# Kernel optimization log

Measured on AMD Instinct MI355X. Metric: run time of the kernel, lower is better.

Reference implementation:

```python
import jax, jax.numpy as jnp
import numpy as np

B, E, H = 16384, 1024, 1024


def setup_inputs() -> dict:
    key = jax.random.key(0)
    ks = jax.random.split(key, 8)
    s = 1.0 / np.sqrt(H)
    return {
        "x": jax.random.normal(ks[0], (B, E), dtype=jnp.float32),
        "h": jax.random.normal(ks[1], (B, H), dtype=jnp.float32),
        "W_ri": jax.random.normal(ks[2], (E, H), dtype=jnp.float32) * s,
        "b_ri": jnp.zeros((H,), dtype=jnp.float32),
        "W_rh": jax.random.normal(ks[3], (H, H), dtype=jnp.float32) * s,
        "W_zi": jax.random.normal(ks[4], (E, H), dtype=jnp.float32) * s,
        "b_zi": jnp.zeros((H,), dtype=jnp.float32),
        "W_zh": jax.random.normal(ks[5], (H, H), dtype=jnp.float32) * s,
        "W_hi": jax.random.normal(ks[6], (E, H), dtype=jnp.float32) * s,
        "b_hi": jnp.zeros((H,), dtype=jnp.float32),
        "W_hh": jax.random.normal(ks[7], (H, H), dtype=jnp.float32) * s,
    }


def reference(x, h, W_ri, b_ri, W_rh, W_zi, b_zi, W_zh, W_hi, b_hi, W_hh):
    # GRU cell: r/z gates then candidate htilde, then blend.
    rt = jax.nn.sigmoid(x @ W_ri + b_ri + h @ W_rh)          # [B,H]
    zt = jax.nn.sigmoid(x @ W_zi + b_zi + h @ W_zh)          # [B,H]
    htilde = jnp.tanh(x @ W_hi + b_hi + (h * rt) @ W_hh)     # [B,H]
    h_new = (1.0 - zt) * h + zt * htilde                     # [B,H]
    # dp_keep_prob=1.0 -> dropout is identity; module returns (dropout(h), h)
    return h_new
```

## Files before the change

### kernel.cpp

```cpp
#include <hip/hip_runtime.h>


typedef short bf16x8 __attribute__((ext_vector_type(8)));
typedef float f32x4 __attribute__((ext_vector_type(4)));

static __device__ __forceinline__ unsigned short f2bf(float f) {
    unsigned int u = __float_as_uint(f);
    return (unsigned short)((u + 0x7fffu + ((u >> 16) & 1u)) >> 16);
}
static __device__ __forceinline__ float bf2f(unsigned short s) {
    return __uint_as_float(((unsigned int)s) << 16);
}

__global__ void cast2_f32_bf16(const float* __restrict__ a,
                               const float* __restrict__ b,
                               unsigned short* __restrict__ da,
                               unsigned short* __restrict__ db, int n) {
    int i = (blockIdx.x * blockDim.x + threadIdx.x) * 4;
    const float* s;
    unsigned short* d;
    int off;
    if (i < n) { s = a; d = da; off = i; }
    else       { s = b; d = db; off = i - n; }
    float4 v = *(const float4*)(s + off);
    ushort4 o;
    o.x = f2bf(v.x); o.y = f2bf(v.y); o.z = f2bf(v.z); o.w = f2bf(v.w);
    *(ushort4*)(d + off) = o;
}

struct TPlan {
    const float* src[6];
    unsigned short* dst[6];
};
__global__ void transpose_cast6(TPlan p) {
    __shared__ float t[32][33];
    const float* src = p.src[blockIdx.z];
    unsigned short* dst = p.dst[blockIdx.z];
    int bx = blockIdx.x, by = blockIdx.y;
    int tx = threadIdx.x, ty = threadIdx.y;
#pragma unroll
    for (int i = 0; i < 4; ++i)
        t[ty + 8 * i][tx] = src[(by * 32 + ty + 8 * i) * 1024 + bx * 32 + tx];
    __syncthreads();
#pragma unroll
    for (int i = 0; i < 4; ++i) {
        int n = bx * 32 + ty + 8 * i;
        int k = by * 32 + tx;
        dst[n * 2048 + k] = f2bf(t[tx][ty + 8 * i]);
    }
}

template <int MODE, int NBN_LOG>
__global__ void gemm_gru(const unsigned short* __restrict__ Alo,
                         const unsigned short* __restrict__ Ahi,
                         const unsigned short* __restrict__ Bt,
                         const float* __restrict__ bias_z,
                         const float* __restrict__ bias_r,
                         const unsigned short* __restrict__ hb,
                         const unsigned short* __restrict__ ztb_in,
                         const float* __restrict__ hf,
                         unsigned short* __restrict__ ztb_out,
                         unsigned short* __restrict__ ab_out,
                         float* __restrict__ out) {
    constexpr int NBN = 1 << NBN_LOG;
    __shared__ __attribute__((aligned(16))) short As[128 * 32];
    __shared__ __attribute__((aligned(16))) short Bs[128 * 32];

    const int t = threadIdx.x;
    const int lane = t & 63;
    const int wave = t >> 6;
    const int i = blockIdx.x;
    const int bml = i & 7;
    const int bn = (i >> 3) & (NBN - 1);
    const int bmg = i >> (3 + NBN_LOG);
    const int bm = bmg * 8 + bml;
    const int wm = wave >> 1, wn = wave & 1;

    f32x4 acc[4][4] = {};

    const int rowA0 = bm * 128;
    const int rowB0 = bn * 128;
    const int koff = (lane >> 4) * 8;
    const int rsub = lane & 15;

    const short* Ap[4];
    const short* Bp[4];
#pragma unroll
    for (int mi = 0; mi < 4; ++mi)
        Ap[mi] = As + (wm * 64 + mi * 16 + rsub) * 32 + koff;
#pragma unroll
    for (int ni = 0; ni < 4; ++ni)
        Bp[ni] = Bs + (wn * 64 + ni * 16 + rsub) * 32 + koff;

    for (int half = 0; half < 2; ++half) {
        const unsigned short* Ab = (half ? Ahi : Alo) + rowA0 * 1024;
        const unsigned short* Bb = Bt + rowB0 * 2048 + half * 1024;
        for (int kk = 0; kk < 1024; kk += 32) {
            const unsigned short* Asrc = Ab + kk;
            const unsigned short* Bsrc = Bb + kk;

            __syncthreads();
#pragma unroll
            for (int j = 0; j < 2; ++j) {
                int c = j * 256 + wave * 64 + lane;
                int row = c >> 2, part = c & 3;
                __builtin_amdgcn_global_load_lds(
                    (const __attribute__((address_space(1))) void*)(Asrc + row * 1024 + part * 8),
                    (__attribute__((address_space(3))) void*)(As + (j * 256 + wave * 64) * 8),
                    16, 0, 0);
                __builtin_amdgcn_global_load_lds(
                    (const __attribute__((address_space(1))) void*)(Bsrc + row * 2048 + part * 8),
                    (__attribute__((address_space(3))) void*)(Bs + (j * 256 + wave * 64) * 8),
                    16, 0, 0);
            }
            __syncthreads();

            bf16x8 af[4], bfr[4];
#pragma unroll
            for (int mi = 0; mi < 4; ++mi) af[mi] = *(const bf16x8*)Ap[mi];
#pragma unroll
            for (int ni = 0; ni < 4; ++ni) bfr[ni] = *(const bf16x8*)Bp[ni];
#pragma unroll
            for (int mi = 0; mi < 4; ++mi)
#pragma unroll
                for (int ni = 0; ni < 4; ++ni)
                    acc[mi][ni] = __builtin_amdgcn_mfma_f32_16x16x32_bf16(
                        af[mi], bfr[ni], acc[mi][ni], 0, 0, 0);
        }
    }

    const int q = lane >> 4;
#pragma unroll
    for (int mi = 0; mi < 4; ++mi) {
#pragma unroll
        for (int ni = 0; ni < 4; ++ni) {
            int colg = bn * 128 + wn * 64 + ni * 16 + rsub;
            int row0 = bm * 128 + wm * 64 + mi * 16 + q * 4;
            if (MODE == 0) {
                bool isZ = colg < 1024;
                int col = colg & 1023;
                float bz = isZ ? bias_z[col] : bias_r[col];
#pragma unroll
                for (int r = 0; r < 4; ++r) {
                    int idx = (row0 + r) * 1024 + col;
                    float v = acc[mi][ni][r] + bz;
                    float s = 1.0f / (1.0f + __expf(-v));
                    if (isZ) ztb_out[idx] = f2bf(s);
                    else     ab_out[idx] = f2bf(bf2f(hb[idx]) * s);
                }
            } else {
                int col = colg;
                float bz = bias_z[col];
#pragma unroll
                for (int r = 0; r < 4; ++r) {
                    int idx = (row0 + r) * 1024 + col;
                    float v = acc[mi][ni][r] + bz;
                    float e = __expf(2.0f * v);
                    float ht = 1.0f - 2.0f / (e + 1.0f);
                    float hv = hf[idx];
                    float z = bf2f(ztb_in[idx]);
                    out[idx] = fmaf(z, ht - hv, hv);
                }
            }
        }
    }
}

extern "C" void kernel_launch(void* const* d_in, const int* in_sizes, int n_in,
                              void* d_out, int out_size, void* d_ws, size_t ws_size,
                              hipStream_t stream) {
    const float* x    = (const float*)d_in[0];
    const float* h    = (const float*)d_in[1];
    const float* W_ri = (const float*)d_in[2];
    const float* b_ri = (const float*)d_in[3];
    const float* W_rh = (const float*)d_in[4];
    const float* W_zi = (const float*)d_in[5];
    const float* b_zi = (const float*)d_in[6];
    const float* W_zh = (const float*)d_in[7];
    const float* W_hi = (const float*)d_in[8];
    const float* b_hi = (const float*)d_in[9];
    const float* W_hh = (const float*)d_in[10];
    float* out = (float*)d_out;

    const size_t MB = 1024ull * 1024ull;
    char* ws = (char*)d_ws;
    unsigned short* xb   = (unsigned short*)(ws);
    unsigned short* hb   = (unsigned short*)(ws + 32 * MB);
    unsigned short* ab   = (unsigned short*)(ws + 64 * MB);
    unsigned short* ztb  = (unsigned short*)(ws + 96 * MB);
    unsigned short* Bzr  = (unsigned short*)(ws + 128 * MB);
    unsigned short* Bh   = (unsigned short*)(ws + 136 * MB);

    const int NELEM = 16384 * 1024;
    cast2_f32_bf16<<<2 * NELEM / (256 * 4), 256, 0, stream>>>(x, h, xb, hb, NELEM);

    TPlan p;
    p.src[0] = W_zi; p.dst[0] = Bzr + 0 * 2048 + 0;
    p.src[1] = W_zh; p.dst[1] = Bzr + 0 * 2048 + 1024;
    p.src[2] = W_ri; p.dst[2] = Bzr + 1024 * 2048 + 0;
    p.src[3] = W_rh; p.dst[3] = Bzr + 1024 * 2048 + 1024;
    p.src[4] = W_hi; p.dst[4] = Bh + 0;
    p.src[5] = W_hh; p.dst[5] = Bh + 1024;
    transpose_cast6<<<dim3(32, 32, 6), dim3(32, 8), 0, stream>>>(p);

    gemm_gru<0, 4><<<2048, 256, 0, stream>>>(xb, hb, Bzr, b_zi, b_ri,
                                             hb, nullptr, nullptr,
                                             ztb, ab, nullptr);
    gemm_gru<1, 3><<<1024, 256, 0, stream>>>(xb, ab, Bh, b_hi, nullptr,
                                             nullptr, ztb, h,
                                             nullptr, nullptr, out);
}
```

Measured before the change: 491.4 us.

## Rewrite GRU GEMMs with 256x256 tiles, double-buffered LDS pipeline and swizzle

Both GEMM kernels move from 128x128 tiles with 256 threads to 256x256 tiles with 512 threads (8 waves, each computing 128x64). Global-to-LDS loads are double-buffered and interleaved with MFMA phases under explicit vmcnt waits and barriers. The LDS layout is XOR-swizzled to avoid bank conflicts, and s_setprio is raised around the MFMA runs. The aim is to hide memory latency and raise data reuse per tile. In exchange the kernels use more LDS and registers and launch fewer blocks (512 and 256), which may leave some CUs underfilled.

```diff
diff --git a/kernel.cpp b/kernel.cpp
--- a/kernel.cpp
+++ b/kernel.cpp
@@ -3,6 +3,8 @@
 
 typedef short bf16x8 __attribute__((ext_vector_type(8)));
 typedef float f32x4 __attribute__((ext_vector_type(4)));
+
+template <int V> struct Ic { static constexpr int value = V; };
 
 static __device__ __forceinline__ unsigned short f2bf(float f) {
     unsigned int u = __float_as_uint(f);
@@ -51,91 +53,141 @@
 }
 
 template <int MODE, int NBN_LOG>
-__global__ void gemm_gru(const unsigned short* __restrict__ Alo,
-                         const unsigned short* __restrict__ Ahi,
-                         const unsigned short* __restrict__ Bt,
-                         const float* __restrict__ bias_z,
-                         const float* __restrict__ bias_r,
-                         const unsigned short* __restrict__ hb,
-                         const unsigned short* __restrict__ ztb_in,
-                         const float* __restrict__ hf,
-                         unsigned short* __restrict__ ztb_out,
-                         unsigned short* __restrict__ ab_out,
-                         float* __restrict__ out) {
+__global__ __launch_bounds__(512, 2) void gemm_gru(
+        const unsigned short* __restrict__ Alo,
+        const unsigned short* __restrict__ Ahi,
+        const unsigned short* __restrict__ Bt,
+        const float* __restrict__ bias_z,
+        const float* __restrict__ bias_r,
+        const unsigned short* __restrict__ hb,
+        const unsigned short* __restrict__ ztb_in,
+        const float* __restrict__ hf,
+        unsigned short* __restrict__ ztb_out,
+        unsigned short* __restrict__ ab_out,
+        float* __restrict__ out) {
     constexpr int NBN = 1 << NBN_LOG;
-    __shared__ __attribute__((aligned(16))) short As[128 * 32];
-    __shared__ __attribute__((aligned(16))) short Bs[128 * 32];
+    constexpr int NT = 32;
+    __shared__ __attribute__((aligned(16))) short As[2][2][256 * 32];
+    __shared__ __attribute__((aligned(16))) short Bs[2][2][256 * 32];
 
     const int t = threadIdx.x;
     const int lane = t & 63;
     const int wave = t >> 6;
+    const int wm = wave >> 2, wn = wave & 3;
+
     const int i = blockIdx.x;
     const int bml = i & 7;
     const int bn = (i >> 3) & (NBN - 1);
     const int bmg = i >> (3 + NBN_LOG);
     const int bm = bmg * 8 + bml;
-    const int wm = wave >> 1, wn = wave & 1;
-
-    f32x4 acc[4][4] = {};
-
-    const int rowA0 = bm * 128;
-    const int rowB0 = bn * 128;
-    const int koff = (lane >> 4) * 8;
-    const int rsub = lane & 15;
-
-    const short* Ap[4];
-    const short* Bp[4];
-#pragma unroll
-    for (int mi = 0; mi < 4; ++mi)
-        Ap[mi] = As + (wm * 64 + mi * 16 + rsub) * 32 + koff;
-#pragma unroll
-    for (int ni = 0; ni < 4; ++ni)
-        Bp[ni] = Bs + (wn * 64 + ni * 16 + rsub) * 32 + koff;
-
-    for (int half = 0; half < 2; ++half) {
-        const unsigned short* Ab = (half ? Ahi : Alo) + rowA0 * 1024;
-        const unsigned short* Bb = Bt + rowB0 * 2048 + half * 1024;
-        for (int kk = 0; kk < 1024; kk += 32) {
-            const unsigned short* Asrc = Ab + kk;
-            const unsigned short* Bsrc = Bb + kk;
-
-            __syncthreads();
-#pragma unroll
-            for (int j = 0; j < 2; ++j) {
-                int c = j * 256 + wave * 64 + lane;
-                int row = c >> 2, part = c & 3;
-                __builtin_amdgcn_global_load_lds(
-                    (const __attribute__((address_space(1))) void*)(Asrc + row * 1024 + part * 8),
-                    (__attribute__((address_space(3))) void*)(As + (j * 256 + wave * 64) * 8),
-                    16, 0, 0);
-                __builtin_amdgcn_global_load_lds(
-                    (const __attribute__((address_space(1))) void*)(Bsrc + row * 2048 + part * 8),
-                    (__attribute__((address_space(3))) void*)(Bs + (j * 256 + wave * 64) * 8),
-                    16, 0, 0);
-            }
-            __syncthreads();
-
-            bf16x8 af[4], bfr[4];
-#pragma unroll
-            for (int mi = 0; mi < 4; ++mi) af[mi] = *(const bf16x8*)Ap[mi];
-#pragma unroll
-            for (int ni = 0; ni < 4; ++ni) bfr[ni] = *(const bf16x8*)Bp[ni];
-#pragma unroll
-            for (int mi = 0; mi < 4; ++mi)
-#pragma unroll
-                for (int ni = 0; ni < 4; ++ni)
-                    acc[mi][ni] = __builtin_amdgcn_mfma_f32_16x16x32_bf16(
-                        af[mi], bfr[ni], acc[mi][ni], 0, 0, 0);
-        }
+
+    const int l4 = lane & 15, kg = lane >> 4;
+    const int rdcol = ((kg ^ ((l4 >> 1) & 3)) * 8);
+    const int aoff = (wm * 128 + l4) * 32 + rdcol;
+    const int boff = (wn * 64 + l4) * 32 + rdcol;
+
+    const int srow = t >> 2;
+    const int scol = (((t & 3) ^ ((t >> 3) & 3)) * 8);
+    const int rowA0 = bm * 256;
+    const int rowB0 = bn * 256;
+
+    f32x4 acc[8][4] = {};
+    bf16x8 bfr[4];
+
+    auto stage_half = [&](const unsigned short* src, int stride, int grow0,
+                          int kcol, short* dst) {
+#pragma unroll
+        for (int j = 0; j < 2; ++j) {
+            const unsigned short* g =
+                src + (size_t)(grow0 + j * 128 + srow) * stride + (kcol + scol);
+            __builtin_amdgcn_global_load_lds(
+                (const __attribute__((address_space(1))) void*)g,
+                (__attribute__((address_space(3))) void*)(dst + (j * 512 + wave * 64) * 8),
+                16, 0, 0);
+        }
+    };
+    auto stage_A = [&](int T, int s) {
+        const unsigned short* Ab = (T < 16) ? Alo : Ahi;
+        stage_half(Ab, 1024, rowA0, ((T * 64) & 1023) + s * 32, &As[T & 1][s][0]);
+    };
+    auto stage_B = [&](int T, int s) {
+        stage_half(Bt, 2048, rowB0, T * 64 + s * 32, &Bs[T & 1][s][0]);
+    };
+
+    auto nop = [] {};
+    auto vm4 = [] { asm volatile("s_waitcnt vmcnt(4)" ::: "memory"); };
+    auto vm0 = [] { asm volatile("s_waitcnt vmcnt(0)" ::: "memory"); };
+
+    auto phase = [&](auto dC, auto mC, auto sC, auto stage, auto vmw) {
+        constexpr int d = decltype(dC)::value;
+        constexpr int m0 = decltype(mC)::value;
+        constexpr int s = decltype(sC)::value;
+        const short* Ab = &As[d][s][aoff];
+        const short* Bb = &Bs[d][s][boff];
+        bf16x8 af0 = *(const bf16x8*)(Ab + (m0 + 0) * 512);
+        bf16x8 af1 = *(const bf16x8*)(Ab + (m0 + 1) * 512);
+        bf16x8 af2 = *(const bf16x8*)(Ab + (m0 + 2) * 512);
+        bf16x8 af3 = *(const bf16x8*)(Ab + (m0 + 3) * 512);
+        if constexpr (m0 == 0) {
+#pragma unroll
+            for (int ni = 0; ni < 4; ++ni)
+                bfr[ni] = *(const bf16x8*)(Bb + ni * 512);
+        }
+        stage();
+        __builtin_amdgcn_s_barrier();
+        asm volatile("s_waitcnt lgkmcnt(0)" ::: "memory");
+        __builtin_amdgcn_s_setprio(1);
+#pragma unroll
+        for (int ni = 0; ni < 4; ++ni) {
+            acc[m0 + 0][ni] = __builtin_amdgcn_mfma_f32_16x16x32_bf16(
+                af0, bfr[ni], acc[m0 + 0][ni], 0, 0, 0);
+            acc[m0 + 1][ni] = __builtin_amdgcn_mfma_f32_16x16x32_bf16(
+                af1, bfr[ni], acc[m0 + 1][ni], 0, 0, 0);
+        }
+#pragma unroll
+        for (int ni = 0; ni < 4; ++ni) {
+            acc[m0 + 2][ni] = __builtin_amdgcn_mfma_f32_16x16x32_bf16(
+                af2, bfr[ni], acc[m0 + 2][ni], 0, 0, 0);
+            acc[m0 + 3][ni] = __builtin_amdgcn_mfma_f32_16x16x32_bf16(
+                af3, bfr[ni], acc[m0 + 3][ni], 0, 0, 0);
+        }
+        __builtin_amdgcn_s_setprio(0);
+        vmw();
+        __builtin_amdgcn_s_barrier();
+    };
+
+    stage_A(0, 0); stage_B(0, 0); stage_A(0, 1); stage_B(0, 1);
+    stage_A(1, 0); stage_B(1, 0);
+    asm volatile("s_waitcnt vmcnt(4)" ::: "memory");
+    __builtin_amdgcn_s_barrier();
+
+    auto tile = [&](auto dC, int kt) {
+        phase(dC, Ic<0>{}, Ic<0>{}, [&] { stage_A(kt + 1, 1); }, nop);
+        phase(dC, Ic<4>{}, Ic<0>{}, [&] { stage_B(kt + 1, 1); }, vm4);
+        phase(dC, Ic<0>{}, Ic<1>{}, [&] { stage_A(kt + 2, 0); }, nop);
+        phase(dC, Ic<4>{}, Ic<1>{}, [&] { stage_B(kt + 2, 0); }, vm4);
+    };
+
+    for (int kt = 0; kt < NT - 2; kt += 2) {
+        tile(Ic<0>{}, kt);
+        tile(Ic<1>{}, kt + 1);
     }
-
-    const int q = lane >> 4;
-#pragma unroll
-    for (int mi = 0; mi < 4; ++mi) {
+    phase(Ic<0>{}, Ic<0>{}, Ic<0>{}, [&] { stage_A(NT - 1, 1); }, nop);
+    phase(Ic<0>{}, Ic<4>{}, Ic<0>{}, [&] { stage_B(NT - 1, 1); }, vm4);
+    phase(Ic<0>{}, Ic<0>{}, Ic<1>{}, nop, nop);
+    phase(Ic<0>{}, Ic<4>{}, Ic<1>{}, nop, vm0);
+    phase(Ic<1>{}, Ic<0>{}, Ic<0>{}, nop, nop);
+    phase(Ic<1>{}, Ic<4>{}, Ic<0>{}, nop, nop);
+    phase(Ic<1>{}, Ic<0>{}, Ic<1>{}, nop, nop);
+    phase(Ic<1>{}, Ic<4>{}, Ic<1>{}, nop, nop);
+
+    const int q4 = kg * 4;
+#pragma unroll
+    for (int mi = 0; mi < 8; ++mi) {
+        int row0 = bm * 256 + wm * 128 + mi * 16 + q4;
 #pragma unroll
         for (int ni = 0; ni < 4; ++ni) {
-            int colg = bn * 128 + wn * 64 + ni * 16 + rsub;
-            int row0 = bm * 128 + wm * 64 + mi * 16 + q * 4;
+            int colg = bn * 256 + wn * 64 + ni * 16 + l4;
             if (MODE == 0) {
                 bool isZ = colg < 1024;
                 int col = colg & 1023;
@@ -149,11 +201,10 @@
                     else     ab_out[idx] = f2bf(bf2f(hb[idx]) * s);
                 }
             } else {
-                int col = colg;
-                float bz = bias_z[col];
+                float bz = bias_z[colg];
 #pragma unroll
                 for (int r = 0; r < 4; ++r) {
-                    int idx = (row0 + r) * 1024 + col;
+                    int idx = (row0 + r) * 1024 + colg;
                     float v = acc[mi][ni][r] + bz;
                     float e = __expf(2.0f * v);
                     float ht = 1.0f - 2.0f / (e + 1.0f);
@@ -203,10 +254,10 @@
     p.src[5] = W_hh; p.dst[5] = Bh + 1024;
     transpose_cast6<<<dim3(32, 32, 6), dim3(32, 8), 0, stream>>>(p);
 
-    gemm_gru<0, 4><<<2048, 256, 0, stream>>>(xb, hb, Bzr, b_zi, b_ri,
-                                             hb, nullptr, nullptr,
-                                             ztb, ab, nullptr);
-    gemm_gru<1, 3><<<1024, 256, 0, stream>>>(xb, ab, Bh, b_hi, nullptr,
-                                             nullptr, ztb, h,
-                                             nullptr, nullptr, out);
-}
+    gemm_gru<0, 3><<<512, 512, 0, stream>>>(xb, hb, Bzr, b_zi, b_ri,
+                                            hb, nullptr, nullptr,
+                                            ztb, ab, nullptr);
+    gemm_gru<1, 2><<<256, 512, 0, stream>>>(xb, ab, Bh, b_hi, nullptr,
+                                            nullptr, ztb, h,
+                                            nullptr, nullptr, out);
+}
```

Result: faster. 466.2 us (-5.1%).
